# Kernel optimization log

Hardware: AMD Instinct MI355X
Metric: run time of the kernel (lower is better)

Reference implementation:

```python
import jax, jax.numpy as jnp
import numpy as np

B, S = 65536, 128          # batch of tasks, support set size
MAX_CLASSES = 10
STATS_DIM = MAX_CLASSES + 4  # hist + [n_nonzero, entropy, subset_size, hist_max]
TOKEN_DIM = 256


def setup_inputs() -> dict:
    key = jax.random.key(0)
    k1, k2, k3, k4, k5 = jax.random.split(key, 5)
    y_support = jax.random.randint(k1, (B, S), 0, MAX_CLASSES, dtype=jnp.int32)
    # MLP params: Linear(14, D) -> GELU -> Linear(D, D)
    w1 = jax.random.normal(k2, (STATS_DIM, TOKEN_DIM), jnp.float32) / np.sqrt(STATS_DIM)
    b1 = jax.random.normal(k3, (TOKEN_DIM,), jnp.float32) * 0.01
    w2 = jax.random.normal(k4, (TOKEN_DIM, TOKEN_DIM), jnp.float32) / np.sqrt(TOKEN_DIM)
    b2 = jax.random.normal(k5, (TOKEN_DIM,), jnp.float32) * 0.01
    return {"y_support": y_support, "w1": w1, "b1": b1, "w2": w2, "b2": b2}


def reference(y_support, w1, b1, w2, b2):
    b, s = y_support.shape
    # Batched bincount via scatter-add: hist[i, c] = #{j : y_support[i, j] == c}
    rows = jnp.arange(b, dtype=jnp.int32)[:, None]              # [B, 1]
    hist = jnp.zeros((b, MAX_CLASSES), jnp.float32).at[rows, y_support].add(1.0)
    total = jnp.maximum(hist.sum(axis=-1, keepdims=True), 1.0)  # clamp_min(1.0)
    p = hist / total                                            # [B, C]
    entropy = -(p * jnp.log(p + 1e-6)).sum(axis=-1)             # [B]
    n_nonzero = (p > 0).sum(axis=-1).astype(jnp.float32)        # [B]
    stats = jnp.concatenate([
        p,
        n_nonzero[:, None],
        entropy[:, None],
        jnp.full((b, 1), float(s), jnp.float32),
        p.max(axis=-1, keepdims=True),
    ], axis=1)                                                  # [B, C+4]
    h = jax.nn.gelu(stats @ w1 + b1, approximate=False)         # exact GELU like nn.GELU
    return h @ w2 + b2                                          # [B, TOKEN_DIM]
```

## Files before the change

kernel.cpp:

```cpp
#include <hip/hip_runtime.h>
#include <stdint.h>


#define SSUP 128
#define DD   256

typedef __attribute__((ext_vector_type(8)))  short bf16x8;
typedef __attribute__((ext_vector_type(16))) float f32x16;

__device__ __forceinline__ unsigned f2bf_u(float f) {
    union { float f; unsigned u; } v; v.f = f;
    return (v.u + 0x7FFFu + ((v.u >> 16) & 1u)) >> 16;
}
__device__ __forceinline__ unsigned pk2(float a, float b) {
    return f2bf_u(a) | (f2bf_u(b) << 16);
}

__device__ __forceinline__ float gelu_f(float x) {
    float z = 0.7978845608028654f * x * (1.0f + 0.044715f * x * x);
    float e = __expf(-2.0f * z);
    float th = 2.0f / (1.0f + e) - 1.0f;
    return 0.5f * x * (1.0f + th);
}

__global__ void prep_kernel(const float* __restrict__ w1,
                            const float* __restrict__ w2,
                            unsigned short* __restrict__ w1t,
                            unsigned short* __restrict__ w2t) {
    int tid = blockIdx.x * 256 + threadIdx.x;
    if (tid < DD * DD) {
        int n = tid >> 8, k = tid & 255;
        w2t[tid] = (unsigned short)f2bf_u(w2[k * DD + n]);
    } else {
        int t = tid - DD * DD;
        int n = t >> 4, kk = t & 15;
        w1t[t] = (kk < 14) ? (unsigned short)f2bf_u(w1[kk * DD + n])
                           : (unsigned short)0;
    }
}

__global__ __launch_bounds__(256, 4)
void encoder_kernel(const int* __restrict__ y,
                    const float* __restrict__ b1,
                    const float* __restrict__ b2,
                    const unsigned short* __restrict__ w1t,
                    const unsigned short* __restrict__ w2t,
                    float* __restrict__ out) {
    __shared__ __align__(16) unsigned short stats_a[64][16];
    __shared__ __align__(16) unsigned short h_lds[64][264];

    const int tid = threadIdx.x;
    const int r0 = blockIdx.x * 64;

    const int rl = tid >> 2;
    const int q  = tid & 3;
    const int4* yp = (const int4*)(y + (size_t)(r0 + rl) * SSUP + q * 32);
    unsigned long long pkc = 0ull;
    #pragma unroll
    for (int i = 0; i < 8; ++i) {
        int4 v = yp[i];
        pkc += 1ull << (6 * v.x);
        pkc += 1ull << (6 * v.y);
        pkc += 1ull << (6 * v.z);
        pkc += 1ull << (6 * v.w);
    }
    float p[10]; float ent = 0.f, pmax = 0.f, nnz = 0.f;
    #pragma unroll
    for (int c = 0; c < 10; ++c) {
        int cc = (int)((pkc >> (6 * c)) & 63ull);
        cc += __shfl_xor(cc, 1);
        cc += __shfl_xor(cc, 2);
        float pc = (float)cc * 0.0078125f;
        p[c] = pc;
        nnz += (cc > 0) ? 1.0f : 0.0f;
        ent -= pc * __logf(pc + 1e-6f);
        pmax = fmaxf(pmax, pc);
    }
    if (q < 2) {
        unsigned a0, a1, a2, a3;
        if (q == 0) { a0 = pk2(p[0], p[1]); a1 = pk2(p[2], p[3]);
                      a2 = pk2(p[4], p[5]); a3 = pk2(p[6], p[7]); }
        else        { a0 = pk2(p[8], p[9]); a1 = pk2(nnz, ent);
                      a2 = pk2(128.0f, pmax); a3 = 0u; }
        uint4 vv = make_uint4(a0, a1, a2, a3);
        *(uint4*)&stats_a[rl][q * 8] = vv;
    }
    __syncthreads();

    const int lane = tid & 63;
    const int wid  = tid >> 6;
    const int wm   = wid & 1;
    const int wn   = wid >> 1;
    const int l31  = lane & 31;
    const int lh   = lane >> 5;

    bf16x8 af1 = *(const bf16x8*)&stats_a[32 * wm + l31][lh * 8];
    #pragma unroll
    for (int t = 0; t < 4; ++t) {
        const int col = 128 * wn + 32 * t + l31;
        float bias = b1[col];
        f32x16 c;
        #pragma unroll
        for (int r = 0; r < 16; ++r) c[r] = bias;
        bf16x8 bf1 = *(const bf16x8*)&w1t[col * 16 + lh * 8];
        c = __builtin_amdgcn_mfma_f32_32x32x16_bf16(af1, bf1, c, 0, 0, 0);
        #pragma unroll
        for (int r = 0; r < 16; ++r) {
            int row = (r & 3) + 8 * (r >> 2) + 4 * lh;
            h_lds[32 * wm + row][col] = (unsigned short)f2bf_u(gelu_f(c[r]));
        }
    }
    __syncthreads();

    f32x16 acc[4];
    #pragma unroll
    for (int t = 0; t < 4; ++t) {
        float bias = b2[128 * wn + 32 * t + l31];
        #pragma unroll
        for (int r = 0; r < 16; ++r) acc[t][r] = bias;
    }
    #pragma unroll 4
    for (int s = 0; s < 16; ++s) {
        bf16x8 afr = *(const bf16x8*)&h_lds[32 * wm + l31][s * 16 + lh * 8];
        #pragma unroll
        for (int t = 0; t < 4; ++t) {
            const int col = 128 * wn + 32 * t + l31;
            bf16x8 bfr = *(const bf16x8*)&w2t[(size_t)col * DD + s * 16 + lh * 8];
            acc[t] = __builtin_amdgcn_mfma_f32_32x32x16_bf16(afr, bfr, acc[t], 0, 0, 0);
        }
    }
    #pragma unroll
    for (int t = 0; t < 4; ++t) {
        const int col = 128 * wn + 32 * t + l31;
        #pragma unroll
        for (int r = 0; r < 16; ++r) {
            int row = (r & 3) + 8 * (r >> 2) + 4 * lh;
            out[(size_t)(r0 + 32 * wm + row) * DD + col] = acc[t][r];
        }
    }
}

extern "C" void kernel_launch(void* const* d_in, const int* in_sizes, int n_in,
                              void* d_out, int out_size, void* d_ws, size_t ws_size,
                              hipStream_t stream) {
    const int*   y  = (const int*)d_in[0];
    const float* w1 = (const float*)d_in[1];
    const float* b1 = (const float*)d_in[2];
    const float* w2 = (const float*)d_in[3];
    const float* b2 = (const float*)d_in[4];
    float* out = (float*)d_out;

    unsigned short* w2t = (unsigned short*)d_ws;
    unsigned short* w1t = w2t + DD * DD;

    prep_kernel<<<(DD * DD + DD * 16) / 256, 256, 0, stream>>>(w1, w2, w1t, w2t);

    const int nrows = in_sizes[0] / SSUP;
    encoder_kernel<<<nrows / 64, 256, 0, stream>>>(y, b1, b2, w1t, w2t, out);
}
```

Before: 128.2 us.

## Pre-swizzle weights into MFMA fragment order and split GEMM2 into two passes

The prep kernel now writes W1 and W2 as bf16 in per-lane MFMA fragment order, so each lane's B-operand load is one contiguous 16-byte read and a wavefront reads 1 KB contiguously. The second GEMM runs in two passes of two 32x32 tiles instead of four accumulators at once, which lowers register pressure and may help occupancy. The y loads are interleaved across the four quarter-threads so adjacent lanes read adjacent 16-byte chunks. The cost is that each h fragment is read from LDS twice, and the output stores are split into two phases.

Result: faster. 114.8 us (-10.5%).

```diff
diff --git a/kernel.cpp b/kernel.cpp
--- a/kernel.cpp
+++ b/kernel.cpp
@@ -25,17 +25,36 @@
 
 __global__ void prep_kernel(const float* __restrict__ w1,
                             const float* __restrict__ w2,
-                            unsigned short* __restrict__ w1t,
-                            unsigned short* __restrict__ w2t) {
+                            unsigned short* __restrict__ w1f,
+                            unsigned short* __restrict__ w2f) {
     int tid = blockIdx.x * 256 + threadIdx.x;
-    if (tid < DD * DD) {
-        int n = tid >> 8, k = tid & 255;
-        w2t[tid] = (unsigned short)f2bf_u(w2[k * DD + n]);
-    } else {
-        int t = tid - DD * DD;
-        int n = t >> 4, kk = t & 15;
-        w1t[t] = (kk < 14) ? (unsigned short)f2bf_u(w1[kk * DD + n])
-                           : (unsigned short)0;
+    if (tid < 8192) {
+        int l  = tid & 63;
+        int nt = (tid >> 6) & 7;
+        int s  = tid >> 9;
+        int n  = nt * 32 + (l & 31);
+        int k0 = s * 16 + (l >> 5) * 8;
+        unsigned pk[4];
+        #pragma unroll
+        for (int h = 0; h < 4; ++h)
+            pk[h] = pk2(w2[(size_t)(k0 + 2*h) * DD + n],
+                        w2[(size_t)(k0 + 2*h + 1) * DD + n]);
+        *(uint4*)&w2f[(size_t)tid * 8] = make_uint4(pk[0], pk[1], pk[2], pk[3]);
+    } else if (tid < 8704) {
+        int idx = tid - 8192;
+        int l   = idx & 63;
+        int nt  = idx >> 6;
+        int n   = nt * 32 + (l & 31);
+        int kk0 = (l >> 5) * 8;
+        unsigned pk[4];
+        #pragma unroll
+        for (int h = 0; h < 4; ++h) {
+            int ka = kk0 + 2*h, kb = kk0 + 2*h + 1;
+            float fa = (ka < 14) ? w1[(size_t)ka * DD + n] : 0.0f;
+            float fb = (kb < 14) ? w1[(size_t)kb * DD + n] : 0.0f;
+            pk[h] = pk2(fa, fb);
+        }
+        *(uint4*)&w1f[(size_t)idx * 8] = make_uint4(pk[0], pk[1], pk[2], pk[3]);
     }
 }
 
@@ -43,8 +62,8 @@
 void encoder_kernel(const int* __restrict__ y,
                     const float* __restrict__ b1,
                     const float* __restrict__ b2,
-                    const unsigned short* __restrict__ w1t,
-                    const unsigned short* __restrict__ w2t,
+                    const unsigned short* __restrict__ w1f,
+                    const unsigned short* __restrict__ w2f,
                     float* __restrict__ out) {
     __shared__ __align__(16) unsigned short stats_a[64][16];
     __shared__ __align__(16) unsigned short h_lds[64][264];
@@ -54,11 +73,11 @@
 
     const int rl = tid >> 2;
     const int q  = tid & 3;
-    const int4* yp = (const int4*)(y + (size_t)(r0 + rl) * SSUP + q * 32);
+    const int4* yp = (const int4*)(y + (size_t)(r0 + rl) * SSUP);
     unsigned long long pkc = 0ull;
     #pragma unroll
     for (int i = 0; i < 8; ++i) {
-        int4 v = yp[i];
+        int4 v = yp[i * 4 + q];
         pkc += 1ull << (6 * v.x);
         pkc += 1ull << (6 * v.y);
         pkc += 1ull << (6 * v.z);
@@ -82,8 +101,7 @@
                       a2 = pk2(p[4], p[5]); a3 = pk2(p[6], p[7]); }
         else        { a0 = pk2(p[8], p[9]); a1 = pk2(nnz, ent);
                       a2 = pk2(128.0f, pmax); a3 = 0u; }
-        uint4 vv = make_uint4(a0, a1, a2, a3);
-        *(uint4*)&stats_a[rl][q * 8] = vv;
+        *(uint4*)&stats_a[rl][q * 8] = make_uint4(a0, a1, a2, a3);
     }
     __syncthreads();
 
@@ -97,12 +115,13 @@
     bf16x8 af1 = *(const bf16x8*)&stats_a[32 * wm + l31][lh * 8];
     #pragma unroll
     for (int t = 0; t < 4; ++t) {
-        const int col = 128 * wn + 32 * t + l31;
+        const int nt  = wn * 4 + t;
+        const int col = nt * 32 + l31;
         float bias = b1[col];
         f32x16 c;
         #pragma unroll
         for (int r = 0; r < 16; ++r) c[r] = bias;
-        bf16x8 bf1 = *(const bf16x8*)&w1t[col * 16 + lh * 8];
+        bf16x8 bf1 = *(const bf16x8*)&w1f[(size_t)(nt * 64 + lane) * 8];
         c = __builtin_amdgcn_mfma_f32_32x32x16_bf16(af1, bf1, c, 0, 0, 0);
         #pragma unroll
         for (int r = 0; r < 16; ++r) {
@@ -112,30 +131,35 @@
     }
     __syncthreads();
 
-    f32x16 acc[4];
     #pragma unroll
-    for (int t = 0; t < 4; ++t) {
-        float bias = b2[128 * wn + 32 * t + l31];
+    for (int pass = 0; pass < 2; ++pass) {
+        const int t0 = 2 * pass;
+        f32x16 acc[2];
         #pragma unroll
-        for (int r = 0; r < 16; ++r) acc[t][r] = bias;
-    }
-    #pragma unroll 4
-    for (int s = 0; s < 16; ++s) {
-        bf16x8 afr = *(const bf16x8*)&h_lds[32 * wm + l31][s * 16 + lh * 8];
+        for (int u = 0; u < 2; ++u) {
+            float bias = b2[(wn * 4 + t0 + u) * 32 + l31];
+            #pragma unroll
+            for (int r = 0; r < 16; ++r) acc[u][r] = bias;
+        }
         #pragma unroll
-        for (int t = 0; t < 4; ++t) {
-            const int col = 128 * wn + 32 * t + l31;
-            bf16x8 bfr = *(const bf16x8*)&w2t[(size_t)col * DD + s * 16 + lh * 8];
-            acc[t] = __builtin_amdgcn_mfma_f32_32x32x16_bf16(afr, bfr, acc[t], 0, 0, 0);
+        for (int s = 0; s < 16; ++s) {
+            bf16x8 afr = *(const bf16x8*)&h_lds[32 * wm + l31][s * 16 + lh * 8];
+            #pragma unroll
+            for (int u = 0; u < 2; ++u) {
+                const int nt = wn * 4 + t0 + u;
+                bf16x8 bfr = *(const bf16x8*)
+                    &w2f[(size_t)((s * 8 + nt) * 64 + lane) * 8];
+                acc[u] = __builtin_amdgcn_mfma_f32_32x32x16_bf16(afr, bfr, acc[u], 0, 0, 0);
+            }
         }
-    }
-    #pragma unroll
-    for (int t = 0; t < 4; ++t) {
-        const int col = 128 * wn + 32 * t + l31;
         #pragma unroll
-        for (int r = 0; r < 16; ++r) {
-            int row = (r & 3) + 8 * (r >> 2) + 4 * lh;
-            out[(size_t)(r0 + 32 * wm + row) * DD + col] = acc[t][r];
+        for (int u = 0; u < 2; ++u) {
+            const int col = (wn * 4 + t0 + u) * 32 + l31;
+            #pragma unroll
+            for (int r = 0; r < 16; ++r) {
+                int row = (r & 3) + 8 * (r >> 2) + 4 * lh;
+                out[(size_t)(r0 + 32 * wm + row) * DD + col] = acc[u][r];
+            }
         }
     }
 }
@@ -150,11 +174,11 @@
     const float* b2 = (const float*)d_in[4];
     float* out = (float*)d_out;
 
-    unsigned short* w2t = (unsigned short*)d_ws;
-    unsigned short* w1t = w2t + DD * DD;
+    unsigned short* w2f = (unsigned short*)d_ws;
+    unsigned short* w1f = w2f + 65536;
 
-    prep_kernel<<<(DD * DD + DD * 16) / 256, 256, 0, stream>>>(w1, w2, w1t, w2t);
+    prep_kernel<<<34, 256, 0, stream>>>(w1, w2, w1f, w2f);
 
     const int nrows = in_sizes[0] / SSUP;
-    encoder_kernel<<<nrows / 64, 256, 0, stream>>>(y, b1, b2, w1t, w2t, out);
+    encoder_kernel<<<nrows / 64, 256, 0, stream>>>(y, b1, b2, w1f, w2f, out);
 }
```
